# Kernel optimization log

Measured on AMD Instinct MI355X. Metric: run time of the kernel, lower is better.

The kernel has to match this reference:

```python
import jax, jax.numpy as jnp
import numpy as np

D_MODEL = 1024
NUM_HEADS = 16
D_HEAD = D_MODEL // NUM_HEADS
NEG_BIG = 10000000000.0  # matches the torch module's -1e10 mask constant


def setup_inputs() -> dict:
    key = jax.random.key(0)
    ks = jax.random.split(key, 9)
    d = D_MODEL
    scale = 1.0 / np.sqrt(d)
    inp = {
        "x": jax.random.normal(ks[0], (2, 2048, d), dtype=jnp.float32),
        "W_q": jax.random.normal(ks[1], (d, d), dtype=jnp.float32) * scale,
        "b_q": jnp.zeros((d,), dtype=jnp.float32),
        "W_k": jax.random.normal(ks[2], (d, d), dtype=jnp.float32) * scale,
        "b_k": jnp.zeros((d,), dtype=jnp.float32),
        "W_v": jax.random.normal(ks[3], (d, d), dtype=jnp.float32) * scale,
        "b_v": jnp.zeros((d,), dtype=jnp.float32),
        "W_o": jax.random.normal(ks[4], (d, d), dtype=jnp.float32) * scale,
        "b_o": jnp.zeros((d,), dtype=jnp.float32),
    }
    return inp


def reference(x, W_q, b_q, W_k, b_k, W_v, b_v, W_o, b_o):
    B, S, d = x.shape
    H, Dh = NUM_HEADS, D_HEAD

    Q = x @ W_q + b_q  # [B,S,d]
    K = x @ W_k + b_k
    V = x @ W_v + b_v

    # split heads: [B,S,d] -> [B,H,S,Dh]
    Qh = Q.reshape(B, S, H, Dh).transpose(0, 2, 1, 3)
    Kh = K.reshape(B, S, H, Dh).transpose(0, 2, 1, 3)
    Vh = V.reshape(B, S, H, Dh).transpose(0, 2, 1, 3)

    scores = jnp.einsum("bhid,bhjd->bhij", Qh, Kh) / jnp.sqrt(
        jnp.asarray(Dh, dtype=x.dtype)
    )

    # causal mask: tril(scores) - 1e10 * (1 - tril_mask)
    causal = jnp.tril(jnp.ones((S, S), dtype=x.dtype))
    scores = scores * causal - NEG_BIG * (1.0 - causal)

    attn = jax.nn.softmax(scores, axis=-1)  # dropout p=0.0 -> identity

    vals = jnp.einsum("bhij,bhjd->bhid", attn, Vh)  # [B,H,S,Dh]
    vals = vals.transpose(0, 2, 1, 3).reshape(B, S, d)

    return vals @ W_o + b_o
```

## Files before the change

### kernel.cpp

```cpp
#include <hip/hip_runtime.h>

typedef unsigned short u16;
typedef __attribute__((ext_vector_type(8))) short short8;
typedef __attribute__((ext_vector_type(4))) short shortx4;
typedef __attribute__((ext_vector_type(4))) float floatx4;

#define S_ 2048
#define D_ 1024
#define DQKV_ 3072
#define H_ 16
#define DH_ 64

#define EXP2F(x) __builtin_amdgcn_exp2f(x)

template <bool B> struct BoolC { static constexpr bool value = B; };

__device__ __forceinline__ float bf2f(u16 x) {
    union { unsigned int u; float f; } v; v.u = ((unsigned int)x) << 16; return v.f;
}
__device__ __forceinline__ u16 f2bf(float f) {
    unsigned int u = __float_as_uint(f);
    return (u16)((u + 0x7fffu + ((u >> 16) & 1u)) >> 16);
}
__device__ __forceinline__ unsigned int cvtpk_bf16(float lo, float hi) {
    unsigned int r;
    asm("v_cvt_pk_bf16_f32 %0, %1, %2" : "=v"(r) : "v"(lo), "v"(hi));
    return r;
}

__device__ __forceinline__ void async16(const void* g, void* l) {
    __builtin_amdgcn_global_load_lds(
        (const __attribute__((address_space(1))) unsigned int*)g,
        (__attribute__((address_space(3))) unsigned int*)l, 16, 0, 0);
}

__global__ __launch_bounds__(256) void prep(const float* __restrict__ x,
                                            const float* __restrict__ Wq, const float* __restrict__ Wk,
                                            const float* __restrict__ Wv, const float* __restrict__ Wo,
                                            u16* __restrict__ xb, u16* __restrict__ Wqkvt, u16* __restrict__ Wot) {
    __shared__ u16 tile[32][33];
    const int z = blockIdx.z;
    const int tx = threadIdx.x, ty = threadIdx.y;
    if (z >= 4) {
        const int t = ty * 32 + tx;
        const size_t bid = (size_t)(z - 4) * 1024 + blockIdx.y * 32 + blockIdx.x;
        const size_t i = (bid * 256 + t) * 4;
        float4 v = *(const float4*)&x[i];
        shortx4 h;
        h[0] = (short)f2bf(v.x); h[1] = (short)f2bf(v.y);
        h[2] = (short)f2bf(v.z); h[3] = (short)f2bf(v.w);
        *(shortx4*)&xb[i] = h;
        return;
    }
    const float* W = (z == 0) ? Wq : (z == 1) ? Wk : (z == 2) ? Wv : Wo;
    u16* dst = (z == 3) ? Wot : (Wqkvt + (size_t)z * D_ * D_);
    const int n0 = blockIdx.x * 32, k0 = blockIdx.y * 32;
#pragma unroll
    for (int r = 0; r < 4; ++r) {
        int k = ty + r * 8;
        tile[k][tx] = f2bf(W[(size_t)(k0 + k) * D_ + n0 + tx]);
    }
    __syncthreads();
#pragma unroll
    for (int r = 0; r < 4; ++r) {
        int n = ty + r * 8;
        dst[(size_t)(n0 + n) * D_ + k0 + tx] = tile[tx][n];
    }
}

__global__ __launch_bounds__(256) void transpose_headV(const u16* __restrict__ QKV, u16* __restrict__ Vt) {
    __shared__ u16 tile[64 * 65];
    const int t = threadIdx.x;
    const int bh = blockIdx.y, b = bh >> 4, h = bh & 15;
    const int s0 = blockIdx.x << 6;
#pragma unroll
    for (int i = 0; i < 16; ++i) {
        int idx = t + (i << 8);
        int s = idx >> 6, d = idx & 63;
        tile[s * 65 + d] = QKV[(size_t)(b * S_ + s0 + s) * DQKV_ + 2048 + h * DH_ + d];
    }
    __syncthreads();
#pragma unroll
    for (int i = 0; i < 16; ++i) {
        int idx = t + (i << 8);
        int d = idx >> 6, p = idx & 63;
        int sk = ((p >> 5) << 5) | (((p >> 2) & 1) << 4) | (((p >> 3) & 3) << 2) | (p & 3);
        Vt[((size_t)bh * DH_ + d) * S_ + s0 + p] = tile[sk * 65 + d];
    }
}

template <int BM, int BN, bool OUTF32>
__global__ __launch_bounds__(256) void gemm_bt(const u16* __restrict__ A, const u16* __restrict__ Bt,
                                               const float* __restrict__ b0, const float* __restrict__ b1,
                                               const float* __restrict__ b2, void* __restrict__ Cp,
                                               int M, int N, int Kd) {
    constexpr int FI = BM / 32, FJ = BN / 32;
    constexpr int LPT = BM / 64 + BN / 64;
    static_assert(LPT == 3 || LPT == 4, "vmcnt immediate must match LPT");
    __shared__ __align__(16) u16 smem[3][(BM + BN) * 32];
    const int t = threadIdx.x;

    const int nwg = gridDim.x * gridDim.y;
    int fid = blockIdx.y * gridDim.x + blockIdx.x;
    if ((nwg & 7) == 0) fid = (fid & 7) * (nwg >> 3) + (fid >> 3);
    const int bx = fid % gridDim.x, by = fid / gridDim.x;
    const int m0 = by * BM, n0 = bx * BN;

    const int w = t >> 6, lane = t & 63;
    const int lr = lane & 15, lg = lane >> 4;
    const int wm = (w >> 1) * (BM / 2), wn = (w & 1) * (BN / 2);
    const int srow = lane >> 2, scol = (lane & 3) << 3;
    floatx4 acc[FI][FJ] = {};

    auto stage = [&](int buf, int k0) {
        u16* As = &smem[buf][0];
        u16* Bs = &smem[buf][BM * 32];
#pragma unroll
        for (int c = 0; c < BM / 64; ++c) {
            int rbase = (w * (BM / 64) + c) * 16;
            async16(&A[(size_t)(m0 + rbase + srow) * Kd + k0 + scol], &As[rbase * 32]);
        }
#pragma unroll
        for (int c = 0; c < BN / 64; ++c) {
            int rbase = (w * (BN / 64) + c) * 16;
            async16(&Bt[(size_t)(n0 + rbase + srow) * Kd + k0 + scol], &Bs[rbase * 32]);
        }
    };

    const int nk = Kd / 32;
    stage(0, 0);
    stage(1, 32);
    for (int kk = 0; kk < nk; ++kk) {
        const int cur = kk % 3;
        if (kk + 1 < nk) {
            if constexpr (LPT == 4) asm volatile("s_waitcnt vmcnt(4)\n\ts_barrier" ::: "memory");
            else                    asm volatile("s_waitcnt vmcnt(3)\n\ts_barrier" ::: "memory");
        } else {
            asm volatile("s_waitcnt vmcnt(0)\n\ts_barrier" ::: "memory");
        }
        if (kk + 2 < nk) stage((kk + 2) % 3, (kk + 2) * 32);
        const u16* As = &smem[cur][0];
        const u16* Bs = &smem[cur][BM * 32];

        short8 af[FI], bfr[FJ];
#pragma unroll
        for (int i = 0; i < FI; ++i) af[i]  = *(const short8*)&As[(wm + i * 16 + lr) * 32 + lg * 8];
#pragma unroll
        for (int j = 0; j < FJ; ++j) bfr[j] = *(const short8*)&Bs[(wn + j * 16 + lr) * 32 + lg * 8];
#pragma unroll
        for (int i = 0; i < FI; ++i)
#pragma unroll
            for (int j = 0; j < FJ; ++j)
                acc[i][j] = __builtin_amdgcn_mfma_f32_16x16x32_bf16(af[i], bfr[j], acc[i][j], 0, 0, 0);
    }

    if (!OUTF32) {
        __syncthreads();
        u16* Cs = &smem[0][0];
#pragma unroll
        for (int j = 0; j < FJ; ++j) {
            int c = wn + j * 16 + lr;
            int col = n0 + c;
            const float* bp = (col < 1024) ? b0 : (col < 2048) ? b1 : b2;
            float bv = bp[col & 1023];
#pragma unroll
            for (int i = 0; i < FI; ++i)
#pragma unroll
                for (int ii = 0; ii < 4; ++ii) {
                    int r = wm + i * 16 + lg * 4 + ii;
                    Cs[r * BN + (c ^ ((r & 15) << 3))] = f2bf(acc[i][j][ii] + bv);
                }
        }
        __syncthreads();
        constexpr int CPR = BN / 8;
        constexpr int ITER = BM * CPR / 256;
#pragma unroll
        for (int it = 0; it < ITER; ++it) {
            int g = it * 256 + t;
            int r = g / CPR, cc = g % CPR;
            short8 vv = *(const short8*)&Cs[r * BN + ((cc * 8) ^ ((r & 15) << 3))];
            *(short8*)((u16*)Cp + (size_t)(m0 + r) * N + n0 + cc * 8) = vv;
        }
    } else {
#pragma unroll
        for (int j = 0; j < FJ; ++j) {
            int col = n0 + wn + j * 16 + lr;
            const float* bp = (col < 1024) ? b0 : (col < 2048) ? b1 : b2;
            float bv = bp[col & 1023];
#pragma unroll
            for (int i = 0; i < FI; ++i) {
                int rb = m0 + wm + i * 16 + lg * 4;
#pragma unroll
                for (int ii = 0; ii < 4; ++ii)
                    ((float*)Cp)[(size_t)(rb + ii) * N + col] = acc[i][j][ii] + bv;
            }
        }
    }
}

__global__ __launch_bounds__(256, 4) void attn_mfma(const u16* __restrict__ QKV, const u16* __restrict__ Vt,
                                                    u16* __restrict__ O) {
    __shared__ __align__(16) u16 KsA[2][64 * 64];
    __shared__ __align__(16) u16 VsA[2][64 * 64];
    const int t = threadIdx.x, w = t >> 6, lane = t & 63;
    const int lr = lane & 15, lg = lane >> 4;
    const int wq = w & 1, wk = w >> 1;
    const int bh = blockIdx.x, b = bh >> 4, h = bh & 15;
    const int ya = blockIdx.y & 7, yb = blockIdx.y >> 3;
    const int a4 = (ya + 4) & 7;
    const int cq = (yb == 0) ? ya : (yb == 1) ? (7 - ya) : (yb == 2) ? a4 : (7 - a4);
    const int qt = (yb << 3) + cq;
    const int q0 = qt << 6;
    const float cs = 0.18033688f;

    const u16* Kb  = QKV + (size_t)b * S_ * DQKV_ + 1024 + h * DH_;
    const u16* Vtb = Vt + (size_t)bh * DH_ * S_;

    const int rb8 = lane >> 3;
    const int cc = ((lane & 7) ^ rb8) << 3;
    const int swz = lr & 7;

    short8 qf[2][2];
#pragma unroll
    for (int qs = 0; qs < 2; ++qs)
#pragma unroll
        for (int ks = 0; ks < 2; ++ks)
            qf[qs][ks] = *(const short8*)&QKV[(size_t)(b * S_ + q0 + wq * 32 + qs * 16 + lr) * DQKV_ +
                                              h * DH_ + ks * 32 + lg * 8];

    floatx4 of[2][4] = {};
    float lsum[2] = {0.f, 0.f};

    auto stage = [&](int buf, int kbase) {
        u16* Kd = &KsA[buf][w * 512];
        u16* Vd = &VsA[buf][w * 512];
        async16(&Kb[(size_t)(kbase + w * 8 + rb8) * DQKV_ + cc], Kd);
        async16(&Kb[(size_t)(kbase + 32 + w * 8 + rb8) * DQKV_ + cc], Kd + 2048);
        async16(&Vtb[(size_t)(w * 8 + rb8) * S_ + kbase + cc], Vd);
        async16(&Vtb[(size_t)(32 + w * 8 + rb8) * S_ + kbase + cc], Vd + 2048);
    };

    stage(0, 0);

    auto body = [&](int kb, auto diagc) {
        constexpr bool DIAG = decltype(diagc)::value;
        const int cur = kb & 1;
        __syncthreads();
        if (kb < qt) stage(cur ^ 1, (kb + 1) << 6);
        const u16* Kc = KsA[cur];
        const u16* Vc = VsA[cur];

        floatx4 sf[2][2] = {};
        __builtin_amdgcn_s_setprio(1);
#pragma unroll
        for (int ks = 0; ks < 2; ++ks)
#pragma unroll
            for (int tt = 0; tt < 2; ++tt) {
                short8 kf = *(const short8*)&Kc[(wk * 32 + tt * 16 + lr) * 64 + ((((ks << 2) + lg) ^ swz) << 3)];
                sf[0][tt] = __builtin_amdgcn_mfma_f32_16x16x32_bf16(kf, qf[0][ks], sf[0][tt], 0, 0, 0);
                sf[1][tt] = __builtin_amdgcn_mfma_f32_16x16x32_bf16(kf, qf[1][ks], sf[1][tt], 0, 0, 0);
            }
        __builtin_amdgcn_s_setprio(0);

        float ev[2][2][4];
#pragma unroll
        for (int qs = 0; qs < 2; ++qs)
#pragma unroll
            for (int tt = 0; tt < 2; ++tt) {
                float s0;
#pragma unroll
                for (int ii = 0; ii < 4; ++ii) {
                    float e = EXP2F(sf[qs][tt][ii] * cs);
                    if (DIAG && (wk * 32 + tt * 16 + lg * 4 + ii > wq * 32 + qs * 16 + lr)) e = 0.f;
                    ev[qs][tt][ii] = e;
                    s0 = (ii == 0) ? e : s0 + e;
                }
                lsum[qs] += s0;
            }

        short8 vfr[4];
#pragma unroll
        for (int ttd = 0; ttd < 4; ++ttd)
            vfr[ttd] = *(const short8*)&Vc[(ttd * 16 + lr) * 64 + ((((wk << 2) + lg) ^ swz) << 3)];
        __builtin_amdgcn_s_setprio(1);
#pragma unroll
        for (int qs = 0; qs < 2; ++qs) {
            union { short8 s; unsigned int u[4]; } pk;
            pk.u[0] = cvtpk_bf16(ev[qs][0][0], ev[qs][0][1]);
            pk.u[1] = cvtpk_bf16(ev[qs][0][2], ev[qs][0][3]);
            pk.u[2] = cvtpk_bf16(ev[qs][1][0], ev[qs][1][1]);
            pk.u[3] = cvtpk_bf16(ev[qs][1][2], ev[qs][1][3]);
#pragma unroll
            for (int ttd = 0; ttd < 4; ++ttd)
                of[qs][ttd] = __builtin_amdgcn_mfma_f32_16x16x32_bf16(pk.s, vfr[ttd], of[qs][ttd], 0, 0, 0);
        }
        __builtin_amdgcn_s_setprio(0);
    };

    for (int kb = 0; kb < qt; ++kb) body(kb, BoolC<false>{});
    body(qt, BoolC<true>{});

    __syncthreads();
    float* mb = (float*)&KsA[0][0];
    float* lb = (float*)&VsA[0][0];
    if (wk == 1) {
        float* mw = mb + wq * 2048;
#pragma unroll
        for (int qs = 0; qs < 2; ++qs)
#pragma unroll
            for (int ttd = 0; ttd < 4; ++ttd)
                *(floatx4*)&mw[(qs * 4 + ttd) * 256 + lane * 4] = of[qs][ttd];
        lb[wq * 128 + lane * 2 + 0] = lsum[0];
        lb[wq * 128 + lane * 2 + 1] = lsum[1];
    }
    __syncthreads();
    if (wk == 0) {
        float* mw = mb + wq * 2048;
#pragma unroll
        for (int qs = 0; qs < 2; ++qs)
#pragma unroll
            for (int ttd = 0; ttd < 4; ++ttd)
                of[qs][ttd] += *(const floatx4*)&mw[(qs * 4 + ttd) * 256 + lane * 4];
        lsum[0] += lb[wq * 128 + lane * 2 + 0];
        lsum[1] += lb[wq * 128 + lane * 2 + 1];

        float rv[2][4];
#pragma unroll
        for (int qs = 0; qs < 2; ++qs) {
            float s = lsum[qs];
            s += __shfl_xor(s, 16);
            s += __shfl_xor(s, 32);
            float rinv = 1.f / s;
#pragma unroll
            for (int ii = 0; ii < 4; ++ii)
                rv[qs][ii] = __shfl(rinv, (lane & 48) | (lg * 4 + ii));
        }
#pragma unroll
        for (int qs = 0; qs < 2; ++qs)
#pragma unroll
            for (int ttd = 0; ttd < 4; ++ttd)
#pragma unroll
                for (int ii = 0; ii < 4; ++ii)
                    O[(size_t)(b * S_ + q0 + wq * 32 + qs * 16 + lg * 4 + ii) * D_ + h * DH_ + ttd * 16 + lr] =
                        f2bf(of[qs][ttd][ii] * rv[qs][ii]);
    }
}

extern "C" void kernel_launch(void* const* d_in, const int* in_sizes, int n_in,
                              void* d_out, int out_size, void* d_ws, size_t ws_size,
                              hipStream_t stream) {
    (void)in_sizes; (void)n_in; (void)out_size; (void)ws_size;
    const float* x  = (const float*)d_in[0];
    const float* Wq = (const float*)d_in[1];
    const float* bq = (const float*)d_in[2];
    const float* Wk = (const float*)d_in[3];
    const float* bk = (const float*)d_in[4];
    const float* Wv = (const float*)d_in[5];
    const float* bv = (const float*)d_in[6];
    const float* Wo = (const float*)d_in[7];
    const float* bo = (const float*)d_in[8];

    u16* ws    = (u16*)d_ws;
    u16* WqkvT = ws;
    u16* WoT   = ws + (size_t)3 * (1 << 20);
    u16* QKV   = ws + (size_t)4 * (1 << 20);
    u16* Vtm   = ws + (size_t)16 * (1 << 20);
    u16* xbf   = ws + (size_t)20 * (1 << 20);
    u16* Am    = ws + (size_t)20 * (1 << 20);

    prep<<<dim3(32, 32, 8), dim3(32, 8), 0, stream>>>(x, Wq, Wk, Wv, Wo, xbf, WqkvT, WoT);

    gemm_bt<128, 128, false><<<dim3(DQKV_ / 128, 4096 / 128), 256, 0, stream>>>(
        xbf, WqkvT, bq, bk, bv, QKV, 4096, DQKV_, 1024);

    transpose_headV<<<dim3(32, 32), 256, 0, stream>>>(QKV, Vtm);

    attn_mfma<<<dim3(32, 32), 256, 0, stream>>>(QKV, Vtm, Am);

    gemm_bt<64, 128, true><<<dim3(1024 / 128, 4096 / 64), 256, 0, stream>>>(
        Am, WoT, bo, bo, bo, d_out, 4096, 1024, 1024);
}
```

Before: 177.1 us.

## Use 256x256-tile 512-thread GEMM with ping-pong scheduling for QKV projection

Replaces the 128x128 QKV projection GEMM with a new 256x256 tile kernel using 8 waves, double-buffered async LDS loads with a K-step of 64, and fragment loads interleaved with MFMA groups separated by barriers and setprio. Larger tiles raise arithmetic intensity and cut global traffic per FLOP. The trade-off is a smaller grid (192 blocks, fewer than the CU count), heavy register pressure from 8x4 accumulators, and large LDS use, which may limit occupancy.

```diff
diff --git a/kernel.cpp b/kernel.cpp
--- a/kernel.cpp
+++ b/kernel.cpp
@@ -12,8 +12,10 @@
 #define DH_ 64
 
 #define EXP2F(x) __builtin_amdgcn_exp2f(x)
+#define SBAR asm volatile("s_barrier" ::: "memory")
 
 template <bool B> struct BoolC { static constexpr bool value = B; };
+template <int I>  struct IntC  { static constexpr int  value = I; };
 
 __device__ __forceinline__ float bf2f(u16 x) {
     union { unsigned int u; float f; } v; v.u = ((unsigned int)x) << 16; return v.f;
@@ -89,6 +91,115 @@
     }
 }
 
+__global__ __launch_bounds__(512, 2) void gemm256(const u16* __restrict__ A, const u16* __restrict__ Bt,
+                                                  const float* __restrict__ b0, const float* __restrict__ b1,
+                                                  const float* __restrict__ b2, u16* __restrict__ Cp,
+                                                  int N, int Kd) {
+    __shared__ __align__(16) u16 smem[2][2 * 256 * 64];
+    const int t = threadIdx.x;
+
+    const int nwg = gridDim.x * gridDim.y;
+    int fid = blockIdx.y * gridDim.x + blockIdx.x;
+    if ((nwg & 7) == 0) fid = (fid & 7) * (nwg >> 3) + (fid >> 3);
+    const int bx = fid % gridDim.x, by = fid / gridDim.x;
+    const int m0 = by * 256, n0 = bx * 256;
+
+    const int w = t >> 6, lane = t & 63;
+    const int lr = lane & 15, lg = lane >> 4;
+    const int wm = (w >> 2) * 128, wn = (w & 3) * 64;
+    const int rb8 = lane >> 3;
+    const int cc = ((lane & 7) ^ rb8) << 3;
+    const int swz = lr & 7;
+
+    floatx4 acc[8][4] = {};
+    short8 af[4][2], bfr[2][2];
+
+    auto stage = [&](int buf, int k0) {
+        u16* As = &smem[buf][0];
+        u16* Bs = &smem[buf][256 * 64];
+#pragma unroll
+        for (int g = 0; g < 4; ++g) {
+            async16(&A[(size_t)(m0 + w * 32 + g * 8 + rb8) * Kd + k0 + cc], &As[(w * 32 + g * 8) * 64]);
+            async16(&Bt[(size_t)(n0 + w * 32 + g * 8 + rb8) * Kd + k0 + cc], &Bs[(w * 32 + g * 8) * 64]);
+        }
+    };
+
+    const int nk = Kd / 64;
+    stage(0, 0);
+    for (int kt = 0; kt < nk; ++kt) {
+        const int cur = kt & 1;
+        asm volatile("s_waitcnt vmcnt(0)\n\ts_barrier" ::: "memory");
+        if (kt + 1 < nk) stage(cur ^ 1, (kt + 1) * 64);
+        const u16* As = &smem[cur][0];
+        const u16* Bs = &smem[cur][256 * 64];
+
+        auto ldA = [&](int rh) {
+#pragma unroll
+            for (int i = 0; i < 4; ++i)
+#pragma unroll
+                for (int ks = 0; ks < 2; ++ks)
+                    af[i][ks] = *(const short8*)&As[(wm + rh * 64 + i * 16 + lr) * 64 +
+                                                    ((((ks << 2) + lg) ^ swz) << 3)];
+        };
+        auto ldB = [&](int ch) {
+#pragma unroll
+            for (int j = 0; j < 2; ++j)
+#pragma unroll
+                for (int ks = 0; ks < 2; ++ks)
+                    bfr[j][ks] = *(const short8*)&Bs[(wn + ch * 32 + j * 16 + lr) * 64 +
+                                                     ((((ks << 2) + lg) ^ swz) << 3)];
+        };
+        auto mm = [&](auto RH, auto CH) {
+            constexpr int rh = RH.value, chv = CH.value;
+            __builtin_amdgcn_s_setprio(1);
+#pragma unroll
+            for (int i = 0; i < 4; ++i)
+#pragma unroll
+                for (int j = 0; j < 2; ++j)
+#pragma unroll
+                    for (int ks = 0; ks < 2; ++ks)
+                        acc[rh * 4 + i][chv * 2 + j] =
+                            __builtin_amdgcn_mfma_f32_16x16x32_bf16(af[i][ks], bfr[j][ks],
+                                                                    acc[rh * 4 + i][chv * 2 + j], 0, 0, 0);
+            __builtin_amdgcn_s_setprio(0);
+        };
+
+        ldA(0); ldB(0);
+        SBAR; mm(IntC<0>{}, IntC<0>{}); SBAR;
+        ldB(1);
+        SBAR; mm(IntC<0>{}, IntC<1>{}); SBAR;
+        ldA(1);
+        SBAR; mm(IntC<1>{}, IntC<1>{}); SBAR;
+        ldB(0);
+        SBAR; mm(IntC<1>{}, IntC<0>{});
+    }
+
+    __syncthreads();
+    u16* Cs = &smem[0][0];
+#pragma unroll
+    for (int j = 0; j < 4; ++j) {
+        int c = wn + j * 16 + lr;
+        int col = n0 + c;
+        const float* bp = (col < 1024) ? b0 : (col < 2048) ? b1 : b2;
+        float bv = bp[col & 1023];
+#pragma unroll
+        for (int i = 0; i < 8; ++i)
+#pragma unroll
+            for (int ii = 0; ii < 4; ++ii) {
+                int r = wm + i * 16 + lg * 4 + ii;
+                Cs[r * 256 + (c ^ ((r & 15) << 3))] = f2bf(acc[i][j][ii] + bv);
+            }
+    }
+    __syncthreads();
+#pragma unroll
+    for (int it = 0; it < 16; ++it) {
+        int g = it * 512 + t;
+        int r = g >> 5, c2 = g & 31;
+        short8 vv = *(const short8*)&Cs[r * 256 + ((c2 * 8) ^ ((r & 15) << 3))];
+        *(short8*)&Cp[(size_t)(m0 + r) * N + n0 + c2 * 8] = vv;
+    }
+}
+
 template <int BM, int BN, bool OUTF32>
 __global__ __launch_bounds__(256) void gemm_bt(const u16* __restrict__ A, const u16* __restrict__ Bt,
                                                const float* __restrict__ b0, const float* __restrict__ b1,
@@ -177,9 +288,9 @@
 #pragma unroll
         for (int it = 0; it < ITER; ++it) {
             int g = it * 256 + t;
-            int r = g / CPR, cc = g % CPR;
-            short8 vv = *(const short8*)&Cs[r * BN + ((cc * 8) ^ ((r & 15) << 3))];
-            *(short8*)((u16*)Cp + (size_t)(m0 + r) * N + n0 + cc * 8) = vv;
+            int r = g / CPR, c3 = g % CPR;
+            short8 vv = *(const short8*)&Cs[r * BN + ((c3 * 8) ^ ((r & 15) << 3))];
+            *(short8*)((u16*)Cp + (size_t)(m0 + r) * N + n0 + c3 * 8) = vv;
         }
     } else {
 #pragma unroll
@@ -370,8 +481,8 @@
 
     prep<<<dim3(32, 32, 8), dim3(32, 8), 0, stream>>>(x, Wq, Wk, Wv, Wo, xbf, WqkvT, WoT);
 
-    gemm_bt<128, 128, false><<<dim3(DQKV_ / 128, 4096 / 128), 256, 0, stream>>>(
-        xbf, WqkvT, bq, bk, bv, QKV, 4096, DQKV_, 1024);
+    gemm256<<<dim3(DQKV_ / 256, 4096 / 256), 512, 0, stream>>>(
+        xbf, WqkvT, bq, bk, bv, QKV, DQKV_, 1024);
 
     transpose_headV<<<dim3(32, 32), 256, 0, stream>>>(QKV, Vtm);
 
```

New measurement: 178.0 us. No clear change (+0.5%).
